# Performance work log

Measured on AMD Instinct MI355X. Metric: run time of the kernel, lower is better.

Reference implementation:

```python
import jax, jax.numpy as jnp
import numpy as np

NUM_HEADS = 16
ROPE_THETA = 10000.0


def _rope_angles(seq_len, head_dim, dtype):
    # lucidrains rotary_embedding_torch: freqs = theta^(-2i/d) for i in 0..d/2,
    # angles = pos * freq, then each angle repeated twice along last dim (interleaved pairs).
    inv_freq = 1.0 / (ROPE_THETA ** (jnp.arange(0, head_dim, 2, dtype=jnp.float32) / head_dim))
    angles = jnp.arange(seq_len, dtype=jnp.float32)[:, None] * inv_freq  # [N, D/2]
    return jnp.repeat(angles, 2, axis=-1).astype(dtype)  # [N, D]


def _rotate_half(t):
    # interleaved pairs: (x0, x1) -> (-x1, x0)
    t1 = t[..., ::2]
    t2 = t[..., 1::2]
    return jnp.stack([-t2, t1], axis=-1).reshape(t.shape)


def _apply_rope(t, cos, sin):
    # t: [B, H, N, D]; cos/sin: [N, D]
    return t * cos + _rotate_half(t) * sin


def setup_inputs() -> dict:
    key = jax.random.key(0)
    ks = jax.random.split(key, 5)
    B, N, C = 4, 1024, 1024
    return {
        "x": jax.random.normal(ks[0], (B, N, C), dtype=jnp.float32),
        "w_qkv": jax.random.normal(ks[1], (C, 3 * C), dtype=jnp.float32) * (C ** -0.5),
        "b_qkv": jax.random.normal(ks[2], (3 * C,), dtype=jnp.float32) * 0.02,
        "w_proj": jax.random.normal(ks[3], (C, C), dtype=jnp.float32) * (C ** -0.5),
        "b_proj": jax.random.normal(ks[4], (C,), dtype=jnp.float32) * 0.02,
    }


def reference(x, w_qkv, b_qkv, w_proj, b_proj):
    B, N, C = x.shape
    H = NUM_HEADS
    D = C // H

    qkv = x @ w_qkv + b_qkv  # [B, N, 3C]
    qkv = qkv.reshape(B, N, 3, H, D).transpose(2, 0, 3, 1, 4)  # [3, B, H, N, D]
    q, k, v = qkv[0], qkv[1], qkv[2]

    ang = _rope_angles(N, D, x.dtype)
    cos, sin = jnp.cos(ang), jnp.sin(ang)
    q = _apply_rope(q, cos, sin)
    k = _apply_rope(k, cos, sin)

    scale = D ** -0.5  # SDPA default scale
    scores = jnp.einsum("bhqd,bhkd->bhqk", q, k) * scale
    attn = jax.nn.softmax(scores, axis=-1)
    out = jnp.einsum("bhqk,bhkd->bhqd", attn, v)  # [B, H, N, D]

    out = out.transpose(0, 2, 1, 3).reshape(B, N, C)
    return out @ w_proj + b_proj
```

## Files before the change

### kernel.cpp

```cpp
#include <hip/hip_runtime.h>
#include <math.h>

#define BB 4
#define NN 1024
#define CC 1024
#define HH 16
#define DD 64
#define N3 3072

typedef __attribute__((ext_vector_type(8))) short bf16x8;
typedef __attribute__((ext_vector_type(8))) _Float16 f16x8;
typedef __attribute__((ext_vector_type(4))) _Float16 f16x4;
typedef __attribute__((ext_vector_type(4))) float f32x4;
typedef __attribute__((ext_vector_type(4))) unsigned int u32x4;
typedef __attribute__((ext_vector_type(2))) unsigned int u32x2;

struct ushort4_t { unsigned short x, y, z, w; };

static __device__ __forceinline__ unsigned short f2b(float f) {
    union { float f; unsigned int u; } v; v.f = f;
    unsigned int r = (v.u + 0x7fffu + ((v.u >> 16) & 1u)) >> 16;
    return (unsigned short)r;
}

static __device__ __forceinline__ void ldg_lds16(const void* g, void* l) {
    __builtin_amdgcn_global_load_lds(
        (const __attribute__((address_space(1))) unsigned int*)g,
        (__attribute__((address_space(3))) unsigned int*)l, 16, 0, 0);
}

static __device__ __forceinline__ void barx()  { asm volatile("s_barrier" ::: "memory"); }
static __device__ __forceinline__ void wlg0()  { asm volatile("s_waitcnt lgkmcnt(0)" ::: "memory");
                                                 __builtin_amdgcn_sched_barrier(0); }
static __device__ __forceinline__ void wvm8()  { asm volatile("s_waitcnt vmcnt(8)" ::: "memory"); }
static __device__ __forceinline__ void wvm4()  { asm volatile("s_waitcnt vmcnt(4)" ::: "memory"); }
static __device__ __forceinline__ void wvm0()  { asm volatile("s_waitcnt vmcnt(0)" ::: "memory"); }
static __device__ __forceinline__ void wnone() {}

__global__ __launch_bounds__(256) void prep(const float* __restrict__ x,
                                            const float* __restrict__ wq,
                                            const float* __restrict__ wp,
                                            _Float16* __restrict__ Xh,
                                            _Float16* __restrict__ Wqt,
                                            _Float16* __restrict__ Wpt,
                                            float* __restrict__ ct,
                                            float* __restrict__ st) {
    __shared__ __align__(16) _Float16 T[64][72];
    const int blk = blockIdx.x;
    const int t = threadIdx.x;
    if (blk < 4096) {
        int tid = blk * 256 + t;
        float4 v = ((const float4*)x)[tid];
        f16x4 o = {(_Float16)v.x, (_Float16)v.y, (_Float16)v.z, (_Float16)v.w};
        ((f16x4*)Xh)[tid] = o;
    } else if (blk < 5120) {
        const float* src; _Float16* dst; int ns, k0, n0;
        if (blk < 4864) {
            int idx = blk - 4096;
            k0 = (idx & 15) * 64; n0 = (idx >> 4) * 64;
            src = wq; dst = Wqt; ns = N3;
        } else {
            int idx = blk - 4864;
            k0 = (idx & 15) * 64; n0 = (idx >> 4) * 64;
            src = wp; dst = Wpt; ns = 1024;
        }
        {
            const int r  = t >> 2;
            const int cf = (t & 3) * 16;
            const float* sp = src + (size_t)(k0 + r) * ns + n0 + cf;
            float4 v0 = *(const float4*)(sp);
            float4 v1 = *(const float4*)(sp + 4);
            float4 v2 = *(const float4*)(sp + 8);
            float4 v3 = *(const float4*)(sp + 12);
            f16x8 a, b;
            a[0]=(_Float16)v0.x; a[1]=(_Float16)v0.y; a[2]=(_Float16)v0.z; a[3]=(_Float16)v0.w;
            a[4]=(_Float16)v1.x; a[5]=(_Float16)v1.y; a[6]=(_Float16)v1.z; a[7]=(_Float16)v1.w;
            b[0]=(_Float16)v2.x; b[1]=(_Float16)v2.y; b[2]=(_Float16)v2.z; b[3]=(_Float16)v2.w;
            b[4]=(_Float16)v3.x; b[5]=(_Float16)v3.y; b[6]=(_Float16)v3.z; b[7]=(_Float16)v3.w;
            *(f16x8*)&T[r][cf]     = a;
            *(f16x8*)&T[r][cf + 8] = b;
        }
        __syncthreads();
        {
            const int n  = t >> 2;
            const int kc = t & 3;
            f16x8 o0, o1;
            #pragma unroll
            for (int kk = 0; kk < 8; kk++) o0[kk] = T[kc * 16 + kk][n];
            #pragma unroll
            for (int kk = 0; kk < 8; kk++) o1[kk] = T[kc * 16 + 8 + kk][n];
            _Float16* dp = dst + (size_t)(n0 + n) * 1024 + k0 + kc * 16;
            *(f16x8*)dp       = o0;
            *(f16x8*)(dp + 8) = o1;
        }
    } else {
        int tid = (blk - 5120) * 256 + t;
        int n = tid >> 5, i = tid & 31;
        double ang = (double)n * exp2(-(double)i * (13.287712379549449 / 32.0));
        ct[tid] = (float)cos(ang);
        st[tid] = (float)sin(ang);
    }
}

__global__ __launch_bounds__(512, 2) void qkv_mfma(const _Float16* __restrict__ Ah,
                                                   const _Float16* __restrict__ Bt,
                                                   const float* __restrict__ bias,
                                                   const float* __restrict__ cost,
                                                   const float* __restrict__ sint,
                                                   unsigned short* __restrict__ Q,
                                                   unsigned short* __restrict__ K,
                                                   unsigned short* __restrict__ Vtg) {
    __shared__ __align__(16) _Float16 LA[4][128 * 64];
    __shared__ __align__(16) _Float16 LB[4][128 * 64];

    const int t    = threadIdx.x;
    const int lane = t & 63;
    const int w    = t >> 6;
    const int ln   = lane & 15, qd = lane >> 4;
    const int n0   = blockIdx.x * 256;
    const int m0   = blockIdx.y * 256;
    const int wm   = (w >> 2) * 128;
    const int wn   = (w & 3) * 64;

    const int L0 = t >> 3, hc0 = (t & 7) ^ (L0 & 7);
    const int row0 = 2 * L0 + (hc0 >> 2), co0 = (hc0 & 3) * 16;
    const int pp = 512 + t;
    const int L1 = pp >> 3, hc1 = (pp & 7) ^ (L1 & 7);
    const int row1 = 2 * L1 + (hc1 >> 2), co1 = (hc1 & 3) * 16;

    const char* gA = (const char*)Ah;
    const char* gB = (const char*)Bt;
    const size_t aof0 = (size_t)(m0 + row0) * 2048 + co0;
    const size_t aof1 = (size_t)(m0 + row1) * 2048 + co1;
    const size_t bof0 = (size_t)(n0 + row0) * 2048 + co0;
    const size_t bof1 = (size_t)(n0 + row1) * 2048 + co1;
    const int ld0 = (w * 64) * 8;
    const int ld1 = (512 + w * 64) * 8;

#define STAGE_A(kk, SLOT) { ldg_lds16(gA + aof0 + (size_t)(kk) * 64, &LA[SLOT][ld0]); \
                            ldg_lds16(gA + aof1 + (size_t)(kk) * 64, &LA[SLOT][ld1]); }
#define STAGE_B(kk, SLOT) { ldg_lds16(gB + bof0 + (size_t)(kk) * 64, &LB[SLOT][ld0]); \
                            ldg_lds16(gB + bof1 + (size_t)(kk) * 64, &LB[SLOT][ld1]); }

    STAGE_A(0, 0); STAGE_B(0, 0);
    STAGE_A(1, 1); STAGE_B(1, 1);
    STAGE_A(2, 2); STAGE_B(2, 2);
    wvm8();
    barx();

    f32x4 acc[8][4];
    #pragma unroll
    for (int i = 0; i < 8; i++)
        #pragma unroll
        for (int j = 0; j < 4; j++) acc[i][j] = (f32x4){0.f, 0.f, 0.f, 0.f};

    auto frag = [&](const _Float16* Lb, int r, int c) -> f16x8 {
        int idx = ((r >> 1) << 6) + ((((((r & 1) << 2) | c)) ^ ((r >> 1) & 7)) << 3);
        return *(const f16x8*)&Lb[idx];
    };

#define QK_TILE(kk, SLOT, STG, WAITFN) {                                            \
    const _Float16* Ab = LA[SLOT];                                                  \
    const _Float16* Bb = LB[SLOT];                                                  \
    f16x8 af[4], bf[4];                                                             \
    _Pragma("unroll") for (int i = 0; i < 4; i++) af[i] = frag(Ab, wm + i * 16 + ln, qd); \
    _Pragma("unroll") for (int j = 0; j < 4; j++) bf[j] = frag(Bb, wn + j * 16 + ln, qd); \
    if (STG) STAGE_A((kk) + 3, ((kk) + 3) & 3);                                     \
    barx(); wlg0();                                                                 \
    __builtin_amdgcn_s_setprio(1);                                                  \
    _Pragma("unroll") for (int i = 0; i < 4; i++)                                   \
        _Pragma("unroll") for (int j = 0; j < 4; j++)                               \
            acc[i][j] = __builtin_amdgcn_mfma_f32_16x16x32_f16(af[i], bf[j], acc[i][j], 0, 0, 0); \
    __builtin_amdgcn_s_setprio(0);                                                  \
    barx();                                                                         \
    _Pragma("unroll") for (int i = 0; i < 4; i++) af[i] = frag(Ab, wm + 64 + i * 16 + ln, qd); \
    if (STG) STAGE_B((kk) + 3, ((kk) + 3) & 3);                                     \
    WAITFN();                                                                       \
    barx(); wlg0();                                                                 \
    __builtin_amdgcn_s_setprio(1);                                                  \
    _Pragma("unroll") for (int i = 0; i < 4; i++)                                   \
        _Pragma("unroll") for (int j = 0; j < 4; j++)                               \
            acc[4 + i][j] = __builtin_amdgcn_mfma_f32_16x16x32_f16(af[i], bf[j], acc[4 + i][j], 0, 0, 0); \
    __builtin_amdgcn_s_setprio(0);                                                  \
    barx();                                                                         \
}

    for (int k = 0; k < 28; k += 4) {
        QK_TILE(k + 0, 0, 1, wvm8);
        QK_TILE(k + 1, 1, 1, wvm8);
        QK_TILE(k + 2, 2, 1, wvm8);
        QK_TILE(k + 3, 3, 1, wvm8);
    }
    QK_TILE(28, 0, 1, wvm8);
    QK_TILE(29, 1, 0, wvm4);
    QK_TILE(30, 2, 0, wvm0);
    QK_TILE(31, 3, 0, wnone);

#undef QK_TILE
#undef STAGE_A
#undef STAGE_B

    float* LW = (float*)(&LA[0][0]) + w * (16 * 68);
    const int s = (n0 + wn) >> 10;
    const int h = ((n0 + wn) >> 6) & 15;
    const int erow = lane >> 2;
    const int ec0  = (lane & 3) * 16;

    if (s < 2) {
        unsigned short* dst = (s == 0) ? Q : K;
        const float sc0 = (s == 0) ? 0.125f : 1.0f;
        f32x4 bb0 = *(const f32x4*)&bias[n0 + wn + ec0 + 0];
        f32x4 bb1 = *(const f32x4*)&bias[n0 + wn + ec0 + 4];
        f32x4 bb2 = *(const f32x4*)&bias[n0 + wn + ec0 + 8];
        f32x4 bb3 = *(const f32x4*)&bias[n0 + wn + ec0 + 12];
        #pragma unroll
        for (int i = 0; i < 8; i++) {
            #pragma unroll
            for (int j = 0; j < 4; j++)
                #pragma unroll
                for (int reg = 0; reg < 4; reg++)
                    LW[(qd * 4 + reg) * 68 + j * 16 + ln] = acc[i][j][reg];
            wlg0();
            f32x4 v0 = *(const f32x4*)&LW[erow * 68 + ec0 + 0];
            f32x4 v1 = *(const f32x4*)&LW[erow * 68 + ec0 + 4];
            f32x4 v2 = *(const f32x4*)&LW[erow * 68 + ec0 + 8];
            f32x4 v3 = *(const f32x4*)&LW[erow * 68 + ec0 + 12];
            wlg0();
            int row = m0 + wm + i * 16 + erow;
            int b = row >> 10, n = row & 1023;
            f32x4 cs0 = *(const f32x4*)&cost[n * 32 + (ec0 >> 1)];
            f32x4 cs1 = *(const f32x4*)&cost[n * 32 + (ec0 >> 1) + 4];
            f32x4 sn0 = *(const f32x4*)&sint[n * 32 + (ec0 >> 1)];
            f32x4 sn1 = *(const f32x4*)&sint[n * 32 + (ec0 >> 1) + 4];
            cs0 *= sc0; cs1 *= sc0; sn0 *= sc0; sn1 *= sc0;
            v0 += bb0; v1 += bb1; v2 += bb2; v3 += bb3;
            unsigned int pk0, pk1, pk2, pk3, pk4, pk5, pk6, pk7;
#define RP(PK, ve, vo, cs, sn) { float oe = (ve) * (cs) - (vo) * (sn);              \
                                 float oo = (vo) * (cs) + (ve) * (sn);              \
            asm("v_cvt_pk_bf16_f32 %0, %1, %2" : "=v"(PK) : "v"(oe), "v"(oo)); }
            RP(pk0, v0[0], v0[1], cs0[0], sn0[0]);
            RP(pk1, v0[2], v0[3], cs0[1], sn0[1]);
            RP(pk2, v1[0], v1[1], cs0[2], sn0[2]);
            RP(pk3, v1[2], v1[3], cs0[3], sn0[3]);
            RP(pk4, v2[0], v2[1], cs1[0], sn1[0]);
            RP(pk5, v2[2], v2[3], cs1[1], sn1[1]);
            RP(pk6, v3[0], v3[1], cs1[2], sn1[2]);
            RP(pk7, v3[2], v3[3], cs1[3], sn1[3]);
#undef RP
            unsigned short* op = dst + (((size_t)(b * HH + h)) * NN + n) * DD + ec0;
            u32x4 o0; o0[0] = pk0; o0[1] = pk1; o0[2] = pk2; o0[3] = pk3;
            u32x4 o1; o1[0] = pk4; o1[1] = pk5; o1[2] = pk6; o1[3] = pk7;
            *(u32x4*)op = o0;
            *(u32x4*)(op + 8) = o1;
        }
    } else {
        const float bb = bias[n0 + wn + lane];
        #pragma unroll
        for (int i = 0; i < 8; i++) {
            #pragma unroll
            for (int j = 0; j < 4; j++)
                #pragma unroll
                for (int reg = 0; reg < 4; reg++)
                    LW[(qd * 4 + reg) * 68 + j * 16 + ln] = acc[i][j][reg];
            wlg0();
            float e0  = LW[ 0 * 68 + lane] + bb, e1  = LW[ 1 * 68 + lane] + bb;
            float e2  = LW[ 2 * 68 + lane] + bb, e3  = LW[ 3 * 68 + lane] + bb;
            float e4  = LW[ 4 * 68 + lane] + bb, e5  = LW[ 5 * 68 + lane] + bb;
            float e6  = LW[ 6 * 68 + lane] + bb, e7  = LW[ 7 * 68 + lane] + bb;
            float e8  = LW[ 8 * 68 + lane] + bb, e9  = LW[ 9 * 68 + lane] + bb;
            float e10 = LW[10 * 68 + lane] + bb, e11 = LW[11 * 68 + lane] + bb;
            float e12 = LW[12 * 68 + lane] + bb, e13 = LW[13 * 68 + lane] + bb;
            float e14 = LW[14 * 68 + lane] + bb, e15 = LW[15 * 68 + lane] + bb;
            wlg0();
            unsigned int pk0, pk1, pk2, pk3, pk4, pk5, pk6, pk7;
#define CV(PK, a, b_) asm("v_cvt_pk_bf16_f32 %0, %1, %2" : "=v"(PK) : "v"(a), "v"(b_))
            CV(pk0, e0,  e1);  CV(pk1, e2,  e3);
            CV(pk2, e4,  e5);  CV(pk3, e6,  e7);
            CV(pk4, e8,  e9);  CV(pk5, e10, e11);
            CV(pk6, e12, e13); CV(pk7, e14, e15);
#undef CV
            int row0v = m0 + wm + i * 16;
            int b = row0v >> 10, nn = row0v & 1023;
            unsigned short* vp = Vtg + ((size_t)(b * HH + h) * DD + lane) * NN + nn;
            u32x4 o0; o0[0] = pk0; o0[1] = pk1; o0[2] = pk2; o0[3] = pk3;
            u32x4 o1; o1[0] = pk4; o1[1] = pk5; o1[2] = pk6; o1[3] = pk7;
            *(u32x4*)vp = o0;
            *(u32x4*)(vp + 8) = o1;
        }
    }
}

static __device__ __forceinline__ void gemm_body_pipe_n64(const char* gA, const char* gB,
                                                          int m0, int n0,
                                                          _Float16* As0, _Float16* As1,
                                                          _Float16* Bs0, _Float16* Bs1,
                                                          int tid, int ln, int qd,
                                                          int wm, int wn, f32x4 acc[4][2]) {
    const int lrow   = tid >> 3;
    const int lchunk = tid & 7;
    const int swz    = (lchunk ^ (lrow & 7)) * 8;

    u32x4 pa[4], pb[2];

    #pragma unroll
    for (int c = 0; c < 4; c++)
        pa[c] = *(const u32x4*)(gA + (size_t)(m0 + c * 32 + lrow) * 2048 + lchunk * 16);
    #pragma unroll
    for (int c = 0; c < 2; c++)
        pb[c] = *(const u32x4*)(gB + (size_t)(n0 + c * 32 + lrow) * 2048 + lchunk * 16);
    #pragma unroll
    for (int c = 0; c < 4; c++)
        *(u32x4*)&As0[(c * 32 + lrow) * 64 + swz] = pa[c];
    #pragma unroll
    for (int c = 0; c < 2; c++)
        *(u32x4*)&Bs0[(c * 32 + lrow) * 64 + swz] = pb[c];
    #pragma unroll
    for (int c = 0; c < 4; c++)
        pa[c] = *(const u32x4*)(gA + (size_t)(m0 + c * 32 + lrow) * 2048 + 128 + lchunk * 16);
    #pragma unroll
    for (int c = 0; c < 2; c++)
        pb[c] = *(const u32x4*)(gB + (size_t)(n0 + c * 32 + lrow) * 2048 + 128 + lchunk * 16);
    __syncthreads();

    #pragma unroll
    for (int t = 0; t < 16; t++) {
        const _Float16* Ac = (t & 1) ? As1 : As0;
        const _Float16* Bc = (t & 1) ? Bs1 : Bs0;

        #pragma unroll
        for (int kc = 0; kc < 2; kc++) {
            f16x8 af[4], bf[2];
            #pragma unroll
            for (int i = 0; i < 4; i++)
                af[i] = *(const f16x8*)&Ac[(wm + i * 16 + ln) * 64 +
                                           (((kc * 4 + qd) ^ (ln & 7)) * 8)];
            #pragma unroll
            for (int j = 0; j < 2; j++)
                bf[j] = *(const f16x8*)&Bc[(wn + j * 16 + ln) * 64 +
                                           (((kc * 4 + qd) ^ (ln & 7)) * 8)];
            #pragma unroll
            for (int i = 0; i < 4; i++)
                #pragma unroll
                for (int j = 0; j < 2; j++)
                    acc[i][j] = __builtin_amdgcn_mfma_f32_16x16x32_f16(af[i], bf[j],
                                                                       acc[i][j], 0, 0, 0);
        }

        if (t < 15) {
            _Float16* An = (t & 1) ? As0 : As1;
            _Float16* Bn = (t & 1) ? Bs0 : Bs1;
            #pragma unroll
            for (int c = 0; c < 4; c++)
                *(u32x4*)&An[(c * 32 + lrow) * 64 + swz] = pa[c];
            #pragma unroll
            for (int c = 0; c < 2; c++)
                *(u32x4*)&Bn[(c * 32 + lrow) * 64 + swz] = pb[c];
            if (t < 14) {
                size_t ko = (size_t)(t + 2) * 128;
                #pragma unroll
                for (int c = 0; c < 4; c++)
                    pa[c] = *(const u32x4*)(gA + (size_t)(m0 + c * 32 + lrow) * 2048 + ko + lchunk * 16);
                #pragma unroll
                for (int c = 0; c < 2; c++)
                    pb[c] = *(const u32x4*)(gB + (size_t)(n0 + c * 32 + lrow) * 2048 + ko + lchunk * 16);
            }
        }
        __syncthreads();
    }
}

__global__ __launch_bounds__(256) void attn_flash(const unsigned short* __restrict__ Qb,
                                                  const unsigned short* __restrict__ Kb,
                                                  const unsigned short* __restrict__ Vtg,
                                                  _Float16* __restrict__ AO) {
    __shared__ __align__(16) unsigned short Ks[3][64 * 64];
    __shared__ __align__(16) unsigned short Vt[2][64 * 64];
    __shared__ __align__(16) unsigned short Ps[4][32 * 64];

    const int t    = threadIdx.x;
    const int lane = t & 63;
    const int w    = t >> 6;
    const int ln   = lane & 15;
    const int qd   = lane >> 4;
    const int bq   = blockIdx.x;
    const int h    = blockIdx.y;
    const int b    = blockIdx.z;
    const size_t base = (size_t)(b * HH + h) * NN * DD;
    const char* Kc = (const char*)(Kb + base);
    const char* Vc = (const char*)(Vtg + base);
    const int xorc = ((lane & 7) ^ (lane >> 3)) * 16;
    const int r8   = lane >> 3;
    const int wrow = w * 16;

    bf16x8 qf[2][2];
    #pragma unroll
    for (int g = 0; g < 2; g++) {
        const unsigned short* qp = Qb + base +
            (size_t)(bq * 128 + w * 32 + g * 16 + ln) * DD + qd * 8;
        qf[g][0] = *(const bf16x8*)qp;
        qf[g][1] = *(const bf16x8*)(qp + 32);
    }

    f32x4 o[2][5];
    #pragma unroll
    for (int g = 0; g < 2; g++)
        #pragma unroll
        for (int x = 0; x < 5; x++) o[g][x] = (f32x4){0.f, 0.f, 0.f, 0.f};

    bf16x8 onesf;
    #pragma unroll
    for (int x = 0; x < 8; x++) onesf[x] = (short)0x3F80;

    #pragma unroll
    for (int tile = 0; tile < 3; tile++)
        #pragma unroll
        for (int c = 0; c < 2; c++) {
            int rr = wrow + c * 8 + r8;
            ldg_lds16(Kc + (size_t)(tile * 64 + rr) * 128 + xorc,
                      &Ks[tile][(wrow + c * 8) * 64]);
        }
    #pragma unroll
    for (int tile = 0; tile < 2; tile++)
        #pragma unroll
        for (int c = 0; c < 2; c++) {
            int rr = wrow + c * 8 + r8;
            ldg_lds16(Vc + (size_t)rr * 2048 + (size_t)tile * 128 + xorc,
                      &Vt[tile][(wrow + c * 8) * 64]);
        }
    __syncthreads();

    f32x4 scur[2][4];
    {
        const unsigned short* KsB = Ks[0];
        #pragma unroll
        for (int j = 0; j < 4; j++) {
            bf16x8 k0f = *(const bf16x8*)&KsB[(ln + 16 * j) * 64 + ((qd ^ (ln & 7)) * 8)];
            bf16x8 k1f = *(const bf16x8*)&KsB[(ln + 16 * j) * 64 + (((4 + qd) ^ (ln & 7)) * 8)];
            #pragma unroll
            for (int g = 0; g < 2; g++) {
                f32x4 sj = {0.f, 0.f, 0.f, 0.f};
                sj = __builtin_amdgcn_mfma_f32_16x16x32_bf16(k0f, qf[g][0], sj, 0, 0, 0);
                sj = __builtin_amdgcn_mfma_f32_16x16x32_bf16(k1f, qf[g][1], sj, 0, 0, 0);
                scur[g][j] = sj;
            }
        }
    }

    const float C1 = 1.44269504f;
    const float C0 = -16.0f * 1.44269504f;
    const int swp = 2 * (ln & 7);

    #pragma unroll
    for (int tt = 0; tt < 16; tt++) {
        f32x4 snext[2][4];
        if (tt < 15) {
            const unsigned short* KsB = Ks[(tt + 1) % 3];
            #pragma unroll
            for (int j = 0; j < 4; j++) {
                bf16x8 k0f = *(const bf16x8*)&KsB[(ln + 16 * j) * 64 + ((qd ^ (ln & 7)) * 8)];
                bf16x8 k1f = *(const bf16x8*)&KsB[(ln + 16 * j) * 64 + (((4 + qd) ^ (ln & 7)) * 8)];
                #pragma unroll
                for (int g = 0; g < 2; g++) {
                    f32x4 sj = {0.f, 0.f, 0.f, 0.f};
                    sj = __builtin_amdgcn_mfma_f32_16x16x32_bf16(k0f, qf[g][0], sj, 0, 0, 0);
                    sj = __builtin_amdgcn_mfma_f32_16x16x32_bf16(k1f, qf[g][1], sj, 0, 0, 0);
                    snext[g][j] = sj;
                }
            }
        }

        unsigned short* PsB = &Ps[w][0];
        #pragma unroll
        for (int g = 0; g < 2; g++) {
            char* rowp = (char*)PsB + (g * 16 + ln) * 128;
            #pragma unroll
            for (int j = 0; j < 4; j++) {
                float p0 = exp2f(fmaf(scur[g][j][0], C1, C0));
                float p1 = exp2f(fmaf(scur[g][j][1], C1, C0));
                float p2 = exp2f(fmaf(scur[g][j][2], C1, C0));
                float p3 = exp2f(fmaf(scur[g][j][3], C1, C0));
                unsigned int lo, hi;
                asm("v_cvt_pk_bf16_f32 %0, %1, %2" : "=v"(lo) : "v"(p0), "v"(p1));
                asm("v_cvt_pk_bf16_f32 %0, %1, %2" : "=v"(hi) : "v"(p2), "v"(p3));
                u32x2 pk; pk[0] = lo; pk[1] = hi;
                *(u32x2*)(rowp + (((4 * j + qd) ^ swp) * 8)) = pk;
            }
        }

        {
            const unsigned short* VtB = Vt[tt & 1];
            bf16x8 pf[2][2];
            #pragma unroll
            for (int g = 0; g < 2; g++) {
                pf[g][0] = *(const bf16x8*)&PsB[(g * 16 + ln) * 64 + ((qd ^ (ln & 7)) * 8)];
                pf[g][1] = *(const bf16x8*)&PsB[(g * 16 + ln) * 64 + (((4 + qd) ^ (ln & 7)) * 8)];
            }
            #pragma unroll
            for (int j = 0; j < 4; j++) {
                bf16x8 v0f = *(const bf16x8*)&VtB[(ln + 16 * j) * 64 + ((qd ^ (ln & 7)) * 8)];
                bf16x8 v1f = *(const bf16x8*)&VtB[(ln + 16 * j) * 64 + (((4 + qd) ^ (ln & 7)) * 8)];
                #pragma unroll
                for (int g = 0; g < 2; g++) {
                    o[g][j] = __builtin_amdgcn_mfma_f32_16x16x32_bf16(pf[g][0], v0f, o[g][j], 0, 0, 0);
                    o[g][j] = __builtin_amdgcn_mfma_f32_16x16x32_bf16(pf[g][1], v1f, o[g][j], 0, 0, 0);
                }
            }
            #pragma unroll
            for (int g = 0; g < 2; g++) {
                o[g][4] = __builtin_amdgcn_mfma_f32_16x16x32_bf16(pf[g][0], onesf, o[g][4], 0, 0, 0);
                o[g][4] = __builtin_amdgcn_mfma_f32_16x16x32_bf16(pf[g][1], onesf, o[g][4], 0, 0, 0);
            }
        }

        __syncthreads();

        if (tt <= 12) {
            int tile = tt + 3;
            #pragma unroll
            for (int c = 0; c < 2; c++) {
                int rr = wrow + c * 8 + r8;
                ldg_lds16(Kc + (size_t)(tile * 64 + rr) * 128 + xorc,
                          &Ks[tt % 3][(wrow + c * 8) * 64]);
            }
        }
        if (tt <= 13) {
            int tile = tt + 2;
            #pragma unroll
            for (int c = 0; c < 2; c++) {
                int rr = wrow + c * 8 + r8;
                ldg_lds16(Vc + (size_t)rr * 2048 + (size_t)tile * 128 + xorc,
                          &Vt[tt & 1][(wrow + c * 8) * 64]);
            }
        }

        #pragma unroll
        for (int g = 0; g < 2; g++)
            #pragma unroll
            for (int j = 0; j < 4; j++) scur[g][j] = snext[g][j];
    }

    #pragma unroll
    for (int g = 0; g < 2; g++)
        #pragma unroll
        for (int r = 0; r < 4; r++) {
            float inv = 1.0f / o[g][4][r];
            int q = bq * 128 + w * 32 + g * 16 + qd * 4 + r;
            _Float16* op = AO + (((size_t)b * NN + q) * HH + h) * DD + ln;
            op[0]  = (_Float16)(o[g][0][r] * inv);
            op[16] = (_Float16)(o[g][1][r] * inv);
            op[32] = (_Float16)(o[g][2][r] * inv);
            op[48] = (_Float16)(o[g][3][r] * inv);
        }
}

__global__ __launch_bounds__(256) void proj_mfma(const _Float16* __restrict__ Ah,
                                                 const _Float16* __restrict__ Bt,
                                                 const float* __restrict__ bias,
                                                 float* __restrict__ out) {
    __shared__ __align__(16) _Float16 As[2][128 * 64];
    __shared__ __align__(16) _Float16 Bs[2][64 * 64];
    const int t = threadIdx.x;
    const int lane = t & 63;
    const int w = t >> 6;
    const int ln = lane & 15, qd = lane >> 4;
    const int n0 = blockIdx.x * 64;
    const int m0 = blockIdx.y * 128;
    const int wm = (w >> 1) * 64, wn = (w & 1) * 32;

    f32x4 acc[4][2];
    #pragma unroll
    for (int i = 0; i < 4; i++)
        #pragma unroll
        for (int j = 0; j < 2; j++) acc[i][j] = (f32x4){0.f, 0.f, 0.f, 0.f};

    gemm_body_pipe_n64((const char*)Ah, (const char*)Bt, m0, n0,
                       As[0], As[1], Bs[0], Bs[1], t, ln, qd, wm, wn, acc);

    #pragma unroll
    for (int i = 0; i < 4; i++) {
        #pragma unroll
        for (int reg = 0; reg < 4; reg++) {
            int row = m0 + wm + i * 16 + qd * 4 + reg;
            #pragma unroll
            for (int j = 0; j < 2; j++) {
                int col = n0 + wn + j * 16 + ln;
                out[(size_t)row * 1024 + col] = acc[i][j][reg] + bias[col];
            }
        }
    }
}

extern "C" void kernel_launch(void* const* d_in, const int* in_sizes, int n_in,
                              void* d_out, int out_size, void* d_ws, size_t ws_size,
                              hipStream_t stream) {
    const float* x      = (const float*)d_in[0];
    const float* w_qkv  = (const float*)d_in[1];
    const float* b_qkv  = (const float*)d_in[2];
    const float* w_proj = (const float*)d_in[3];
    const float* b_proj = (const float*)d_in[4];
    float* out = (float*)d_out;

    char* ws = (char*)d_ws;
    _Float16* Xh   = (_Float16*)(ws);
    _Float16* Wqt  = (_Float16*)(ws + (8u << 20));
    _Float16* Wpt  = (_Float16*)(ws + (14u << 20));
    unsigned short* Q  = (unsigned short*)(ws + (16u << 20));
    unsigned short* K  = (unsigned short*)(ws + (24u << 20));
    unsigned short* Vt = (unsigned short*)(ws + (32u << 20));
    _Float16* AOh  = (_Float16*)(ws + (40u << 20));
    float* cost    = (float*)(ws + (48u << 20));
    float* sint    = (float*)(ws + (48u << 20) + (128u << 10));

    prep<<<5248, 256, 0, stream>>>(x, w_qkv, w_proj, Xh, Wqt, Wpt, cost, sint);
    qkv_mfma<<<dim3(12, 16), 512, 0, stream>>>(Xh, Wqt, b_qkv, cost, sint, Q, K, Vt);
    attn_flash<<<dim3(8, 16, 4), 256, 0, stream>>>(Q, K, Vt, AOh);
    proj_mfma<<<dim3(16, 32), 256, 0, stream>>>(AOh, Wpt, b_proj, out);
}
```

Baseline: 174.9 us.

## Load K/V fragments straight from global into registers in attention kernel

The attention kernel no longer stages K and V tiles through shared memory with barriers. Each lane now loads its MFMA fragments directly from global memory into registers, double-buffering K across iterations. It also remaps the 1D grid so blocks sharing a head are co-scheduled, adds s_setprio around MFMA bursts, and uses raw v_exp/rcp instructions. This removes LDS traffic and __syncthreads, but each wave now fetches K/V on its own (more global/L2 traffic) and register pressure rises.

```diff
diff --git a/kernel.cpp b/kernel.cpp
--- a/kernel.cpp
+++ b/kernel.cpp
@@ -369,12 +369,10 @@
     }
 }
 
-__global__ __launch_bounds__(256) void attn_flash(const unsigned short* __restrict__ Qb,
-                                                  const unsigned short* __restrict__ Kb,
-                                                  const unsigned short* __restrict__ Vtg,
-                                                  _Float16* __restrict__ AO) {
-    __shared__ __align__(16) unsigned short Ks[3][64 * 64];
-    __shared__ __align__(16) unsigned short Vt[2][64 * 64];
+__global__ __launch_bounds__(256, 2) void attn_flash(const unsigned short* __restrict__ Qb,
+                                                     const unsigned short* __restrict__ Kb,
+                                                     const unsigned short* __restrict__ Vtg,
+                                                     _Float16* __restrict__ AO) {
     __shared__ __align__(16) unsigned short Ps[4][32 * 64];
 
     const int t    = threadIdx.x;
@@ -382,15 +380,17 @@
     const int w    = t >> 6;
     const int ln   = lane & 15;
     const int qd   = lane >> 4;
-    const int bq   = blockIdx.x;
-    const int h    = blockIdx.y;
-    const int b    = blockIdx.z;
+
+    const int lin  = blockIdx.x;
+    const int slot = lin >> 3;
+    const int hb   = (lin & 7) + 8 * (slot & 7);
+    const int bq   = slot >> 3;
+    const int h    = hb & 15;
+    const int b    = hb >> 4;
+
     const size_t base = (size_t)(b * HH + h) * NN * DD;
     const char* Kc = (const char*)(Kb + base);
     const char* Vc = (const char*)(Vtg + base);
-    const int xorc = ((lane & 7) ^ (lane >> 3)) * 16;
-    const int r8   = lane >> 3;
-    const int wrow = w * 16;
 
     bf16x8 qf[2][2];
     #pragma unroll
@@ -411,74 +411,64 @@
     #pragma unroll
     for (int x = 0; x < 8; x++) onesf[x] = (short)0x3F80;
 
-    #pragma unroll
-    for (int tile = 0; tile < 3; tile++)
-        #pragma unroll
-        for (int c = 0; c < 2; c++) {
-            int rr = wrow + c * 8 + r8;
-            ldg_lds16(Kc + (size_t)(tile * 64 + rr) * 128 + xorc,
-                      &Ks[tile][(wrow + c * 8) * 64]);
-        }
-    #pragma unroll
-    for (int tile = 0; tile < 2; tile++)
-        #pragma unroll
-        for (int c = 0; c < 2; c++) {
-            int rr = wrow + c * 8 + r8;
-            ldg_lds16(Vc + (size_t)rr * 2048 + (size_t)tile * 128 + xorc,
-                      &Vt[tile][(wrow + c * 8) * 64]);
-        }
-    __syncthreads();
-
-    f32x4 scur[2][4];
-    {
-        const unsigned short* KsB = Ks[0];
-        #pragma unroll
-        for (int j = 0; j < 4; j++) {
-            bf16x8 k0f = *(const bf16x8*)&KsB[(ln + 16 * j) * 64 + ((qd ^ (ln & 7)) * 8)];
-            bf16x8 k1f = *(const bf16x8*)&KsB[(ln + 16 * j) * 64 + (((4 + qd) ^ (ln & 7)) * 8)];
-            #pragma unroll
-            for (int g = 0; g < 2; g++) {
-                f32x4 sj = {0.f, 0.f, 0.f, 0.f};
-                sj = __builtin_amdgcn_mfma_f32_16x16x32_bf16(k0f, qf[g][0], sj, 0, 0, 0);
-                sj = __builtin_amdgcn_mfma_f32_16x16x32_bf16(k1f, qf[g][1], sj, 0, 0, 0);
-                scur[g][j] = sj;
-            }
-        }
-    }
+    const char* kbase = Kc + (size_t)ln * 128 + qd * 16;
+    const char* vbase = Vc + (size_t)ln * 2048 + qd * 16;
 
     const float C1 = 1.44269504f;
     const float C0 = -16.0f * 1.44269504f;
     const int swp = 2 * (ln & 7);
-
-    #pragma unroll
-    for (int tt = 0; tt < 16; tt++) {
-        f32x4 snext[2][4];
+    unsigned short* PsB = &Ps[w][0];
+
+    bf16x8 ka[8], kb2[8], va[8];
+    #pragma unroll
+    for (int j = 0; j < 4; j++) {
+        ka[2 * j]     = *(const bf16x8*)(kbase + j * 2048);
+        ka[2 * j + 1] = *(const bf16x8*)(kbase + j * 2048 + 64);
+    }
+
+    auto iter = [&](int tt, bf16x8 (&kc)[8], bf16x8 (&kn)[8]) {
         if (tt < 15) {
-            const unsigned short* KsB = Ks[(tt + 1) % 3];
+            const char* kp = kbase + (size_t)(tt + 1) * 8192;
             #pragma unroll
             for (int j = 0; j < 4; j++) {
-                bf16x8 k0f = *(const bf16x8*)&KsB[(ln + 16 * j) * 64 + ((qd ^ (ln & 7)) * 8)];
-                bf16x8 k1f = *(const bf16x8*)&KsB[(ln + 16 * j) * 64 + (((4 + qd) ^ (ln & 7)) * 8)];
-                #pragma unroll
-                for (int g = 0; g < 2; g++) {
-                    f32x4 sj = {0.f, 0.f, 0.f, 0.f};
-                    sj = __builtin_amdgcn_mfma_f32_16x16x32_bf16(k0f, qf[g][0], sj, 0, 0, 0);
-                    sj = __builtin_amdgcn_mfma_f32_16x16x32_bf16(k1f, qf[g][1], sj, 0, 0, 0);
-                    snext[g][j] = sj;
-                }
-            }
-        }
-
-        unsigned short* PsB = &Ps[w][0];
+                kn[2 * j]     = *(const bf16x8*)(kp + j * 2048);
+                kn[2 * j + 1] = *(const bf16x8*)(kp + j * 2048 + 64);
+            }
+        }
+        {
+            const char* vp = vbase + (size_t)tt * 128;
+            #pragma unroll
+            for (int j = 0; j < 4; j++) {
+                va[2 * j]     = *(const bf16x8*)(vp + (size_t)j * 32768);
+                va[2 * j + 1] = *(const bf16x8*)(vp + (size_t)j * 32768 + 64);
+            }
+        }
+        f32x4 s[2][4];
+        __builtin_amdgcn_s_setprio(1);
+        #pragma unroll
+        for (int j = 0; j < 4; j++)
+            #pragma unroll
+            for (int g = 0; g < 2; g++) {
+                f32x4 sj = {0.f, 0.f, 0.f, 0.f};
+                sj = __builtin_amdgcn_mfma_f32_16x16x32_bf16(kc[2 * j],     qf[g][0], sj, 0, 0, 0);
+                sj = __builtin_amdgcn_mfma_f32_16x16x32_bf16(kc[2 * j + 1], qf[g][1], sj, 0, 0, 0);
+                s[g][j] = sj;
+            }
+        __builtin_amdgcn_s_setprio(0);
         #pragma unroll
         for (int g = 0; g < 2; g++) {
             char* rowp = (char*)PsB + (g * 16 + ln) * 128;
             #pragma unroll
             for (int j = 0; j < 4; j++) {
-                float p0 = exp2f(fmaf(scur[g][j][0], C1, C0));
-                float p1 = exp2f(fmaf(scur[g][j][1], C1, C0));
-                float p2 = exp2f(fmaf(scur[g][j][2], C1, C0));
-                float p3 = exp2f(fmaf(scur[g][j][3], C1, C0));
+                float p0, p1, p2, p3;
+                float x0 = fmaf(s[g][j][0], C1, C0);
+                float x1 = fmaf(s[g][j][1], C1, C0);
+                float x2 = fmaf(s[g][j][2], C1, C0);
+                float x3 = fmaf(s[g][j][3], C1, C0);
+                asm("v_exp_f32 %0, %1" : "=v"(p0) : "v"(x0));
+                asm("v_exp_f32 %0, %1" : "=v"(p1) : "v"(x1));
+                asm("v_exp_f32 %0, %1" : "=v"(p2) : "v"(x2));
+                asm("v_exp_f32 %0, %1" : "=v"(p3) : "v"(x3));
                 unsigned int lo, hi;
                 asm("v_cvt_pk_bf16_f32 %0, %1, %2" : "=v"(lo) : "v"(p0), "v"(p1));
                 asm("v_cvt_pk_bf16_f32 %0, %1, %2" : "=v"(hi) : "v"(p2), "v"(p3));
@@ -486,64 +476,39 @@
                 *(u32x2*)(rowp + (((4 * j + qd) ^ swp) * 8)) = pk;
             }
         }
-
-        {
-            const unsigned short* VtB = Vt[tt & 1];
-            bf16x8 pf[2][2];
+        bf16x8 pf[2][2];
+        #pragma unroll
+        for (int g = 0; g < 2; g++) {
+            pf[g][0] = *(const bf16x8*)&PsB[(g * 16 + ln) * 64 + ((qd ^ (ln & 7)) * 8)];
+            pf[g][1] = *(const bf16x8*)&PsB[(g * 16 + ln) * 64 + (((4 + qd) ^ (ln & 7)) * 8)];
+        }
+        __builtin_amdgcn_s_setprio(1);
+        #pragma unroll
+        for (int j = 0; j < 4; j++)
             #pragma unroll
             for (int g = 0; g < 2; g++) {
-                pf[g][0] = *(const bf16x8*)&PsB[(g * 16 + ln) * 64 + ((qd ^ (ln & 7)) * 8)];
-                pf[g][1] = *(const bf16x8*)&PsB[(g * 16 + ln) * 64 + (((4 + qd) ^ (ln & 7)) * 8)];
-            }
-            #pragma unroll
-            for (int j = 0; j < 4; j++) {
-                bf16x8 v0f = *(const bf16x8*)&VtB[(ln + 16 * j) * 64 + ((qd ^ (ln & 7)) * 8)];
-                bf16x8 v1f = *(const bf16x8*)&VtB[(ln + 16 * j) * 64 + (((4 + qd) ^ (ln & 7)) * 8)];
-                #pragma unroll
-                for (int g = 0; g < 2; g++) {
-                    o[g][j] = __builtin_amdgcn_mfma_f32_16x16x32_bf16(pf[g][0], v0f, o[g][j], 0, 0, 0);
-                    o[g][j] = __builtin_amdgcn_mfma_f32_16x16x32_bf16(pf[g][1], v1f, o[g][j], 0, 0, 0);
-                }
-            }
-            #pragma unroll
-            for (int g = 0; g < 2; g++) {
-                o[g][4] = __builtin_amdgcn_mfma_f32_16x16x32_bf16(pf[g][0], onesf, o[g][4], 0, 0, 0);
-                o[g][4] = __builtin_amdgcn_mfma_f32_16x16x32_bf16(pf[g][1], onesf, o[g][4], 0, 0, 0);
-            }
-        }
-
-        __syncthreads();
-
-        if (tt <= 12) {
-            int tile = tt + 3;
-            #pragma unroll
-            for (int c = 0; c < 2; c++) {
-                int rr = wrow + c * 8 + r8;
-                ldg_lds16(Kc + (size_t)(tile * 64 + rr) * 128 + xorc,
-                          &Ks[tt % 3][(wrow + c * 8) * 64]);
-            }
-        }
-        if (tt <= 13) {
-            int tile = tt + 2;
-            #pragma unroll
-            for (int c = 0; c < 2; c++) {
-                int rr = wrow + c * 8 + r8;
-                ldg_lds16(Vc + (size_t)rr * 2048 + (size_t)tile * 128 + xorc,
-                          &Vt[tt & 1][(wrow + c * 8) * 64]);
-            }
-        }
-
-        #pragma unroll
-        for (int g = 0; g < 2; g++)
-            #pragma unroll
-            for (int j = 0; j < 4; j++) scur[g][j] = snext[g][j];
+                o[g][j] = __builtin_amdgcn_mfma_f32_16x16x32_bf16(pf[g][0], va[2 * j],     o[g][j], 0, 0, 0);
+                o[g][j] = __builtin_amdgcn_mfma_f32_16x16x32_bf16(pf[g][1], va[2 * j + 1], o[g][j], 0, 0, 0);
+            }
+        #pragma unroll
+        for (int g = 0; g < 2; g++) {
+            o[g][4] = __builtin_amdgcn_mfma_f32_16x16x32_bf16(pf[g][0], onesf, o[g][4], 0, 0, 0);
+            o[g][4] = __builtin_amdgcn_mfma_f32_16x16x32_bf16(pf[g][1], onesf, o[g][4], 0, 0, 0);
+        }
+        __builtin_amdgcn_s_setprio(0);
+    };
+
+    #pragma unroll
+    for (int tp = 0; tp < 8; tp++) {
+        iter(2 * tp,     ka,  kb2);
+        iter(2 * tp + 1, kb2, ka);
     }
 
     #pragma unroll
     for (int g = 0; g < 2; g++)
         #pragma unroll
         for (int r = 0; r < 4; r++) {
-            float inv = 1.0f / o[g][4][r];
+            float inv = __builtin_amdgcn_rcpf(o[g][4][r]);
             int q = bq * 128 + w * 32 + g * 16 + qd * 4 + r;
             _Float16* op = AO + (((size_t)b * NN + q) * HH + h) * DD + ln;
             op[0]  = (_Float16)(o[g][0][r] * inv);
@@ -613,6 +578,6 @@
 
     prep<<<5248, 256, 0, stream>>>(x, w_qkv, w_proj, Xh, Wqt, Wpt, cost, sint);
     qkv_mfma<<<dim3(12, 16), 512, 0, stream>>>(Xh, Wqt, b_qkv, cost, sint, Q, K, Vt);
-    attn_flash<<<dim3(8, 16, 4), 256, 0, stream>>>(Q, K, Vt, AOh);
+    attn_flash<<<512, 256, 0, stream>>>(Q, K, Vt, AOh);
     proj_mfma<<<dim3(16, 32), 256, 0, stream>>>(AOh, Wpt, b_proj, out);
 }
```

Result: slower. 196.9 us (+12.6%).
